# Optimization experiments

Measured on AMD Instinct MI355X. Metric: run time of the kernel, lower is better.

The kernel has to match this reference:

```python
import jax, jax.numpy as jnp
import numpy as np

NUM_EMBEDDINGS = 1024
EMBEDDING_DIM = 128
COMMITMENT_COST = 0.25


def setup_inputs() -> dict:
    key = jax.random.key(0)
    k1, k2 = jax.random.split(key)
    z = jax.random.normal(k1, (16, EMBEDDING_DIM, 64, 64), dtype=jnp.float32)
    # torch init: uniform(-1/num_embeddings, 1/num_embeddings)
    lim = 1.0 / NUM_EMBEDDINGS
    embedding = jax.random.uniform(
        k2, (NUM_EMBEDDINGS, EMBEDDING_DIM), dtype=jnp.float32,
        minval=-lim, maxval=lim)
    return {"z": z, "embedding": embedding}


def reference(z, embedding):
    b, c, h, w = z.shape  # c == EMBEDDING_DIM
    # (b, h, w, c) -> (b*h*w, c)
    z_flat = jnp.transpose(z, (0, 2, 3, 1)).reshape(-1, c)
    # squared euclidean distances: ||z||^2 + ||e||^2 - 2 z e^T  -> (N, K)
    distances = (jnp.sum(z_flat ** 2, axis=-1, keepdims=True)
                 + jnp.sum(embedding ** 2, axis=-1)[None, :]
                 - 2.0 * jnp.matmul(z_flat, embedding.T))
    encoding_indices = jnp.argmin(distances, axis=-1)  # (N,) int
    z_q = embedding[encoding_indices].reshape(b, h, w, c)
    z_q = jnp.transpose(z_q, (0, 3, 1, 2))  # (b, c, h, w)
    commitment_loss = COMMITMENT_COST * jnp.sum(
        (jax.lax.stop_gradient(z_q) - z) ** 2)
    codebook_loss = jnp.sum((z_q - jax.lax.stop_gradient(z)) ** 2)
    loss = codebook_loss + commitment_loss
    # straight-through estimator
    z_q_st = z + jax.lax.stop_gradient(z_q - z)
    return (z_q_st, loss, encoding_indices, commitment_loss, codebook_loss)
```

## Files before the change

### kernel.cpp

```cpp
#include <hip/hip_runtime.h>
#include <hip/hip_bf16.h>

#define C 128
#define HW 4096
#define NPOS 65536
#define K 1024
#define MB 128
#define NBLK (NPOS/MB)
#define RS 136
#define RSB 272
#define CHK 64
#define NCH (K/CHK)
#define CHB (CHK*RSB)

#define ZQ_OFF 0
#define LOSS_OFF 8388608
#define IDX_OFF 8388609
#define COMMIT_OFF 8454145
#define CODE_OFF 8454146

#define WS_IMG_OFF 8192

typedef __bf16 bf16x8 __attribute__((ext_vector_type(8)));
typedef float f32x4 __attribute__((ext_vector_type(4)));

__global__ void vq_prep(const float* __restrict__ emb, unsigned char* __restrict__ img,
                        float* __restrict__ S) {
    int k = blockIdx.x;
    int l = threadIdx.x;
    if (k == 0 && l == 0) S[0] = 0.0f;
    float v0 = emb[k * C + l];
    float v1 = emb[k * C + 64 + l];
    __hip_bfloat16 h0 = __float2bfloat16(v0);
    __hip_bfloat16 h1 = __float2bfloat16(v1);
    unsigned short* row = (unsigned short*)(img + (size_t)k * RSB);
    row[l] = *(unsigned short*)&h0;
    row[64 + l] = *(unsigned short*)&h1;
    float s = v0 * v0 + v1 * v1;
    #pragma unroll
    for (int off = 32; off; off >>= 1) s += __shfl_down(s, off);
    if (l == 0) *(float*)(img + (size_t)k * RSB + 256) = s + 1.0f;
}

__global__ __launch_bounds__(256, 2)
void vq_main(const float* __restrict__ z, const float* __restrict__ emb,
             const unsigned char* __restrict__ img,
             float* __restrict__ out, float* __restrict__ S) {
    __shared__ unsigned short zt[MB * RS];
    __shared__ unsigned short bbuf[2][CHK * RS];
    __shared__ unsigned int wbest[2][MB];
    __shared__ unsigned short idxs[MB];
    __shared__ float lred[4];

    const int t = threadIdx.x;
    const int w = t >> 6;
    const int lane = t & 63;
    const int nn = lane & 15;
    const int q = lane >> 4;
    const int wm = w >> 1;
    const int wn = w & 1;

    const int blk = blockIdx.x;
    const int n0g = blk * MB;
    const int b = n0g >> 12;
    const int hw0 = n0g & (HW - 1);
    const float* zg = z + (size_t)b * C * HW + hw0;

    for (int j = w; j < 17; j += 4) {
        __builtin_amdgcn_global_load_lds(
            (const __attribute__((address_space(1))) unsigned int*)(img + j * 1024 + lane * 16),
            (__attribute__((address_space(3))) unsigned int*)((unsigned char*)bbuf[0] + j * 1024),
            16, 0, 0);
    }

    {
        int pos = t & (MB - 1);
        int c0b = (t >> 7) * 64;
        #pragma unroll
        for (int i = 0; i < 16; ++i) {
            int c0 = c0b + i * 4;
            float f0 = zg[(size_t)(c0 + 0) * HW + pos];
            float f1 = zg[(size_t)(c0 + 1) * HW + pos];
            float f2 = zg[(size_t)(c0 + 2) * HW + pos];
            float f3 = zg[(size_t)(c0 + 3) * HW + pos];
            __hip_bfloat16 h0 = __float2bfloat16(f0), h1 = __float2bfloat16(f1),
                           h2 = __float2bfloat16(f2), h3 = __float2bfloat16(f3);
            ushort4 pk;
            pk.x = *(unsigned short*)&h0; pk.y = *(unsigned short*)&h1;
            pk.z = *(unsigned short*)&h2; pk.w = *(unsigned short*)&h3;
            *(ushort4*)&zt[pos * RS + c0] = pk;
        }
    }
    __syncthreads();

    bf16x8 a[4][4];
    #pragma unroll
    for (int mt = 0; mt < 4; ++mt)
        #pragma unroll
        for (int ks = 0; ks < 4; ++ks)
            a[mt][ks] = *(bf16x8*)&zt[(wm * 64 + mt * 16 + nn) * RS + ks * 32 + q * 8];

    unsigned int best[4][4];
    #pragma unroll
    for (int mt = 0; mt < 4; ++mt)
        #pragma unroll
        for (int r = 0; r < 4; ++r) best[mt][r] = 0xFFFFFFFFu;

    for (int ch = 0; ch < NCH; ++ch) {
        const int p = ch & 1;
        if (ch + 1 < NCH) {
            const unsigned char* src = img + (size_t)(ch + 1) * CHB;
            for (int j = w; j < 17; j += 4) {
                __builtin_amdgcn_global_load_lds(
                    (const __attribute__((address_space(1))) unsigned int*)(src + j * 1024 + lane * 16),
                    (__attribute__((address_space(3))) unsigned int*)((unsigned char*)bbuf[p ^ 1] + j * 1024),
                    16, 0, 0);
            }
        }
        const unsigned short* bb = bbuf[p];

        bf16x8 bf[2][4];
        float en[2];
        #pragma unroll
        for (int nt = 0; nt < 2; ++nt) {
            const int row = wn * 32 + nt * 16 + nn;
            #pragma unroll
            for (int ks = 0; ks < 4; ++ks)
                bf[nt][ks] = *(bf16x8*)&bb[row * RS + ks * 32 + q * 8];
            en[nt] = *(const float*)&bb[row * RS + 128];
        }
        const unsigned int code0 = (unsigned int)(ch * CHK + wn * 32 + nn);

        f32x4 acc[4][2];
        #pragma unroll
        for (int mt = 0; mt < 4; ++mt)
            #pragma unroll
            for (int nt = 0; nt < 2; ++nt) acc[mt][nt] = (f32x4){0.f, 0.f, 0.f, 0.f};
        #pragma unroll
        for (int ks = 0; ks < 4; ++ks)
            #pragma unroll
            for (int mt = 0; mt < 4; ++mt)
                #pragma unroll
                for (int nt = 0; nt < 2; ++nt)
                    acc[mt][nt] = __builtin_amdgcn_mfma_f32_16x16x32_bf16(a[mt][ks], bf[nt][ks], acc[mt][nt], 0, 0, 0);

        #pragma unroll
        for (int mt = 0; mt < 4; ++mt)
            #pragma unroll
            for (int r = 0; r < 4; ++r) {
                float s0 = fmaf(acc[mt][0][r], -2.0f, en[0]);
                float s1 = fmaf(acc[mt][1][r], -2.0f, en[1]);
                unsigned int u0 = (__float_as_uint(s0) & ~1023u) | code0;
                unsigned int u1 = (__float_as_uint(s1) & ~1023u) | (code0 + 16u);
                best[mt][r] = min(best[mt][r], min(u0, u1));
            }
        __syncthreads();
    }

    #pragma unroll
    for (int mt = 0; mt < 4; ++mt)
        #pragma unroll
        for (int r = 0; r < 4; ++r) {
            unsigned int v = best[mt][r];
            v = min(v, (unsigned int)__shfl_xor((int)v, 1));
            v = min(v, (unsigned int)__shfl_xor((int)v, 2));
            v = min(v, (unsigned int)__shfl_xor((int)v, 4));
            v = min(v, (unsigned int)__shfl_xor((int)v, 8));
            if (nn == 0) wbest[wn][wm * 64 + mt * 16 + q * 4 + r] = v;
        }
    __syncthreads();

    if (t < MB) {
        unsigned int v = min(wbest[0][t], wbest[1][t]);
        unsigned int code = v & 1023u;
        idxs[t] = (unsigned short)code;
        out[IDX_OFF + n0g + t] = (float)code;
    }
    __syncthreads();

    {
        int pos = t & (MB - 1);
        int c0b = (t >> 7) * 64;
        int myidx = idxs[pos];
        const float* erow = emb + (size_t)myidx * C;
        float* og = out + ZQ_OFF + (size_t)b * C * HW + hw0;
        float ls = 0.f;
        #pragma unroll
        for (int i = 0; i < 16; ++i) {
            int c0 = c0b + i * 4;
            float4 ev = *(const float4*)&erow[c0];
            ushort4 zz = *(ushort4*)&zt[pos * RS + c0];
            float z0 = __uint_as_float((unsigned int)zz.x << 16);
            float z1 = __uint_as_float((unsigned int)zz.y << 16);
            float z2 = __uint_as_float((unsigned int)zz.z << 16);
            float z3 = __uint_as_float((unsigned int)zz.w << 16);
            float d0 = z0 - ev.x, d1 = z1 - ev.y, d2 = z2 - ev.z, d3 = z3 - ev.w;
            ls += d0 * d0 + d1 * d1 + d2 * d2 + d3 * d3;
            og[(size_t)(c0 + 0) * HW + pos] = ev.x;
            og[(size_t)(c0 + 1) * HW + pos] = ev.y;
            og[(size_t)(c0 + 2) * HW + pos] = ev.z;
            og[(size_t)(c0 + 3) * HW + pos] = ev.w;
        }
        #pragma unroll
        for (int off = 32; off; off >>= 1) ls += __shfl_down(ls, off);
        if (lane == 0) lred[w] = ls;
    }
    __syncthreads();
    if (t == 0) atomicAdd(S, lred[0] + lred[1] + lred[2] + lred[3]);
}

__global__ void vq_final(const float* __restrict__ S, float* __restrict__ out) {
    float s = *S;
    out[LOSS_OFF] = 1.25f * s;
    out[COMMIT_OFF] = 0.25f * s;
    out[CODE_OFF] = s;
}

extern "C" void kernel_launch(void* const* d_in, const int* in_sizes, int n_in,
                              void* d_out, int out_size, void* d_ws, size_t ws_size,
                              hipStream_t stream) {
    const float* z = (const float*)d_in[0];
    const float* emb = (const float*)d_in[1];
    float* out = (float*)d_out;
    float* S = (float*)d_ws;
    unsigned char* img = (unsigned char*)d_ws + WS_IMG_OFF;

    vq_prep<<<K, 64, 0, stream>>>(emb, img, S);
    vq_main<<<NBLK, 256, 0, stream>>>(z, emb, img, out, S);
    vq_final<<<1, 1, 0, stream>>>(S, out);
}
```

Baseline: 115.2 us.

## Swizzle codebook layout, split norms to LDS, prefetch two chunks ahead

The codebook image is now packed into unpadded 16KB chunks with an XOR swizzle to avoid LDS bank conflicts, and the norms move to a separate array that is loaded into LDS once. The main loop reads the B fragments into registers, syncs, and then reuses the same buffer to prefetch chunk ch+2, waiting on vmcnt instead of a full __syncthreads. MFMA priority is raised with setprio. The aim is deeper global-to-LDS prefetch and fewer stalls, at the cost of hand-managed waitcnt counts that could race if they are wrong.

```diff
diff --git a/kernel.cpp b/kernel.cpp
--- a/kernel.cpp
+++ b/kernel.cpp
@@ -8,10 +8,10 @@
 #define MB 128
 #define NBLK (NPOS/MB)
 #define RS 136
-#define RSB 272
 #define CHK 64
 #define NCH (K/CHK)
-#define CHB (CHK*RSB)
+#define CHB 16384
+#define NRM_OFF 262144
 
 #define ZQ_OFF 0
 #define LOSS_OFF 8388608
@@ -29,25 +29,28 @@
     int k = blockIdx.x;
     int l = threadIdx.x;
     if (k == 0 && l == 0) S[0] = 0.0f;
-    float v0 = emb[k * C + l];
-    float v1 = emb[k * C + 64 + l];
+    float v0 = emb[k * C + 2 * l];
+    float v1 = emb[k * C + 2 * l + 1];
     __hip_bfloat16 h0 = __float2bfloat16(v0);
     __hip_bfloat16 h1 = __float2bfloat16(v1);
-    unsigned short* row = (unsigned short*)(img + (size_t)k * RSB);
-    row[l] = *(unsigned short*)&h0;
-    row[64 + l] = *(unsigned short*)&h1;
+    unsigned int pk = ((unsigned int)*(unsigned short*)&h1 << 16) | *(unsigned short*)&h0;
+    int r = k & 63;
+    unsigned int lin = (unsigned int)r * 256u + (unsigned int)l * 4u;
+    unsigned int swz = lin ^ ((unsigned int)(r & 7) << 4);
+    *(unsigned int*)(img + (size_t)(k >> 6) * CHB + swz) = pk;
     float s = v0 * v0 + v1 * v1;
     #pragma unroll
     for (int off = 32; off; off >>= 1) s += __shfl_down(s, off);
-    if (l == 0) *(float*)(img + (size_t)k * RSB + 256) = s + 1.0f;
+    if (l == 0) *(float*)(img + NRM_OFF + (size_t)k * 4) = s + 1.0f;
 }
 
 __global__ __launch_bounds__(256, 2)
 void vq_main(const float* __restrict__ z, const float* __restrict__ emb,
              const unsigned char* __restrict__ img,
              float* __restrict__ out, float* __restrict__ S) {
-    __shared__ unsigned short zt[MB * RS];
-    __shared__ unsigned short bbuf[2][CHK * RS];
+    __shared__ __align__(16) unsigned short zt[MB * RS];
+    __shared__ __align__(16) unsigned short bbuf[2][CHB/2];
+    __shared__ __align__(16) float norm_lds[K];
     __shared__ unsigned int wbest[2][MB];
     __shared__ unsigned short idxs[MB];
     __shared__ float lred[4];
@@ -66,10 +69,24 @@
     const int hw0 = n0g & (HW - 1);
     const float* zg = z + (size_t)b * C * HW + hw0;
 
-    for (int j = w; j < 17; j += 4) {
+    #pragma unroll
+    for (int i = 0; i < 4; ++i) {
+        int j = w * 4 + i;
         __builtin_amdgcn_global_load_lds(
             (const __attribute__((address_space(1))) unsigned int*)(img + j * 1024 + lane * 16),
             (__attribute__((address_space(3))) unsigned int*)((unsigned char*)bbuf[0] + j * 1024),
+            16, 0, 0);
+    }
+    __builtin_amdgcn_global_load_lds(
+        (const __attribute__((address_space(1))) unsigned int*)(img + NRM_OFF + w * 1024 + lane * 16),
+        (__attribute__((address_space(3))) unsigned int*)((unsigned char*)norm_lds + w * 1024),
+        16, 0, 0);
+    #pragma unroll
+    for (int i = 0; i < 4; ++i) {
+        int j = w * 4 + i;
+        __builtin_amdgcn_global_load_lds(
+            (const __attribute__((address_space(1))) unsigned int*)(img + CHB + j * 1024 + lane * 16),
+            (__attribute__((address_space(3))) unsigned int*)((unsigned char*)bbuf[1] + j * 1024),
             16, 0, 0);
     }
 
@@ -108,34 +125,43 @@
 
     for (int ch = 0; ch < NCH; ++ch) {
         const int p = ch & 1;
-        if (ch + 1 < NCH) {
-            const unsigned char* src = img + (size_t)(ch + 1) * CHB;
-            for (int j = w; j < 17; j += 4) {
+        const unsigned char* bb = (const unsigned char*)bbuf[p];
+
+        bf16x8 bf[2][4];
+        float en[2];
+        #pragma unroll
+        for (int nt = 0; nt < 2; ++nt) {
+            const int r = wn * 32 + nt * 16 + nn;
+            const unsigned int sx = (unsigned int)(r & 7) << 4;
+            #pragma unroll
+            for (int ks = 0; ks < 4; ++ks)
+                bf[nt][ks] = *(const bf16x8*)(bb + (((unsigned int)r * 256u + ks * 64u + q * 16u) ^ sx));
+            en[nt] = norm_lds[ch * CHK + wn * 32 + nt * 16 + nn];
+        }
+        asm volatile("s_waitcnt lgkmcnt(0)" ::: "memory");
+        __builtin_amdgcn_s_barrier();
+        __builtin_amdgcn_sched_barrier(0);
+
+        if (ch + 2 < NCH) {
+            const unsigned char* src = img + (size_t)(ch + 2) * CHB;
+            #pragma unroll
+            for (int i = 0; i < 4; ++i) {
+                int j = w * 4 + i;
                 __builtin_amdgcn_global_load_lds(
                     (const __attribute__((address_space(1))) unsigned int*)(src + j * 1024 + lane * 16),
-                    (__attribute__((address_space(3))) unsigned int*)((unsigned char*)bbuf[p ^ 1] + j * 1024),
+                    (__attribute__((address_space(3))) unsigned int*)((unsigned char*)bbuf[p] + j * 1024),
                     16, 0, 0);
             }
         }
-        const unsigned short* bb = bbuf[p];
-
-        bf16x8 bf[2][4];
-        float en[2];
-        #pragma unroll
-        for (int nt = 0; nt < 2; ++nt) {
-            const int row = wn * 32 + nt * 16 + nn;
-            #pragma unroll
-            for (int ks = 0; ks < 4; ++ks)
-                bf[nt][ks] = *(bf16x8*)&bb[row * RS + ks * 32 + q * 8];
-            en[nt] = *(const float*)&bb[row * RS + 128];
-        }
+        __builtin_amdgcn_sched_barrier(0);
+
         const unsigned int code0 = (unsigned int)(ch * CHK + wn * 32 + nn);
-
         f32x4 acc[4][2];
         #pragma unroll
         for (int mt = 0; mt < 4; ++mt)
             #pragma unroll
             for (int nt = 0; nt < 2; ++nt) acc[mt][nt] = (f32x4){0.f, 0.f, 0.f, 0.f};
+        __builtin_amdgcn_s_setprio(1);
         #pragma unroll
         for (int ks = 0; ks < 4; ++ks)
             #pragma unroll
@@ -143,6 +169,7 @@
                 #pragma unroll
                 for (int nt = 0; nt < 2; ++nt)
                     acc[mt][nt] = __builtin_amdgcn_mfma_f32_16x16x32_bf16(a[mt][ks], bf[nt][ks], acc[mt][nt], 0, 0, 0);
+        __builtin_amdgcn_s_setprio(0);
 
         #pragma unroll
         for (int mt = 0; mt < 4; ++mt)
@@ -154,7 +181,14 @@
                 unsigned int u1 = (__float_as_uint(s1) & ~1023u) | (code0 + 16u);
                 best[mt][r] = min(best[mt][r], min(u0, u1));
             }
-        __syncthreads();
+
+        if (ch + 2 < NCH) {
+            asm volatile("s_waitcnt vmcnt(4)" ::: "memory");
+        } else {
+            asm volatile("s_waitcnt vmcnt(0)" ::: "memory");
+        }
+        __builtin_amdgcn_s_barrier();
+        __builtin_amdgcn_sched_barrier(0);
     }
 
     #pragma unroll
```

After: 113.4 us. About the same (-1.6%).
